# Kernel tuning notes

Hardware: AMD Instinct MI355X
Metric: run time of the kernel (lower is better)

## Reference

```python
import jax, jax.numpy as jnp
import numpy as np

N = 100000   # nodes
E = 1600000  # edges
B = 64       # graphs
NI, EI, GI = 64, 32, 32   # node_in, edge_in, global_in
NO, EO, GO = 32, 32, 32   # node_out, edge_out, global_out
H = 3                     # attention heads
NEG_SLOPE = 0.2


def setup_inputs() -> dict:
    key = jax.random.key(0)
    ks = jax.random.split(key, 20)
    s = 0.1
    return {
        # graph data
        "x": jax.random.normal(ks[0], (N, NI), jnp.float32),
        "edge_attr": jax.random.normal(ks[1], (E, EI), jnp.float32),
        "glob": jax.random.normal(ks[2], (B, GI), jnp.float32),
        # edge_mlp: Lin(node_in+edge_in, edge_out)
        "W_edge": jax.random.normal(ks[3], (NI + EI, EO), jnp.float32) * s,
        "b_edge": jax.random.normal(ks[4], (EO,), jnp.float32) * s,
        # GATv2Conv params (heads=3, edge_dim=EO)
        "W_l": jax.random.normal(ks[5], (NI, H * NO), jnp.float32) * s,
        "b_l": jax.random.normal(ks[6], (H * NO,), jnp.float32) * s,
        "W_r": jax.random.normal(ks[7], (NI, H * NO), jnp.float32) * s,
        "b_r": jax.random.normal(ks[8], (H * NO,), jnp.float32) * s,
        "W_e": jax.random.normal(ks[9], (EO, H * NO), jnp.float32) * s,   # lin_edge (no bias)
        "att": jax.random.normal(ks[10], (H, NO), jnp.float32) * s,
        "bias_gat": jax.random.normal(ks[11], (H * NO,), jnp.float32) * s,
        # node_mlp_2: Lin(node_out*3 + global_in, node_out)
        "W_n2": jax.random.normal(ks[12], (H * NO + GI, NO), jnp.float32) * s,
        "b_n2": jax.random.normal(ks[13], (NO,), jnp.float32) * s,
        # global_mlp: Lin(global_in + node_out, global_out)
        "W_g": jax.random.normal(ks[14], (GI + NO, GO), jnp.float32) * s,
        "b_g": jax.random.normal(ks[15], (GO,), jnp.float32) * s,
        # int inputs
        "edge_index": jax.random.randint(ks[16], (2, E), 0, N, jnp.int32),
        "batch": jnp.sort(jax.random.randint(ks[17], (N,), 0, B, jnp.int32)),
    }


def reference(x, edge_attr, glob, W_edge, b_edge, W_l, b_l, W_r, b_r, W_e,
              att, bias_gat, W_n2, b_n2, W_g, b_g, edge_index, batch):
    src, dst = edge_index[0], edge_index[1]

    # --- edge model: relu(Lin([x[src], edge_attr])) ---
    e = jax.nn.relu(jnp.concatenate([x[src], edge_attr], axis=1) @ W_edge + b_edge)  # [E, EO]

    # --- node model: GATv2Conv(heads=3, edge_dim=EO), concat heads ---
    xl = (x @ W_l + b_l).reshape(N, H, NO)   # source transform
    xr = (x @ W_r + b_r).reshape(N, H, NO)   # target transform
    m = xl[src] + xr[dst] + (e @ W_e).reshape(E, H, NO)          # [E,H,NO]
    logits = (jax.nn.leaky_relu(m, NEG_SLOPE) * att).sum(-1)     # [E,H]
    # segment softmax over incoming edges of each target node
    mx = jax.ops.segment_max(logits, dst, num_segments=N)        # [N,H]
    ex = jnp.exp(logits - mx[dst])
    den = jax.ops.segment_sum(ex, dst, num_segments=N)           # [N,H]
    alpha = ex / den[dst]                                        # [E,H]
    msg = (alpha[..., None] * xl[src]).reshape(E, H * NO)
    gat_out = jax.ops.segment_sum(msg, dst, num_segments=N) + bias_gat  # [N, H*NO]
    x_new = jax.nn.relu(jnp.concatenate([gat_out, glob[batch]], axis=1) @ W_n2 + b_n2)  # [N,NO]

    # --- global model: relu(Lin([glob, scatter_mean(x_new, batch)])) ---
    cnt = jax.ops.segment_sum(jnp.ones((N,), x.dtype), batch, num_segments=B)
    mean = jax.ops.segment_sum(x_new, batch, num_segments=B) / jnp.maximum(cnt, 1.0)[:, None]
    u_new = jax.nn.relu(jnp.concatenate([glob, mean], axis=1) @ W_g + b_g)  # [B,GO]

    return x_new, e, u_new
```

## Files before the change

### kernel.cpp

```cpp
#include <hip/hip_runtime.h>

#define N_NODES 100000
#define N_EDGES 1600000
#define NB 64
#define NI 64
#define EI 32
#define GI 32
#define NO 32
#define EO 32
#define GO 32
#define HH 3
#define HNO 96
#define NEG 0.2f
#define SCAN_BLKS 98

__global__ __launch_bounds__(256) void kA_node(
    const float* __restrict__ x,
    const float* __restrict__ W_l, const float* __restrict__ b_l,
    const float* __restrict__ W_r, const float* __restrict__ b_r,
    const float* __restrict__ W_edge, const float* __restrict__ b_edge,
    float* __restrict__ xl, float* __restrict__ xr, float* __restrict__ pre_e,
    int niters)
{
    __shared__ float sWl[NI * HNO];
    __shared__ float sWr[NI * HNO];
    __shared__ float sWp[NI * 32];
    __shared__ float sx[64 * NI];
    int t = threadIdx.x;
    for (int f = t; f < NI * HNO; f += 256) { sWl[f] = W_l[f]; sWr[f] = W_r[f]; }
    for (int f = t; f < NI * 32; f += 256) sWp[f] = W_edge[f];
    __syncthreads();
    int k = t & 31, g = t >> 5;
    float bl0 = b_l[k], bl1 = b_l[k + 32], bl2 = b_l[k + 64];
    float br0 = b_r[k], br1 = b_r[k + 32], br2 = b_r[k + 64];
    float bpe = b_edge[k];
    const long NX = (long)N_NODES * NI;
    for (int it = 0; it < niters; ++it) {
        long nb = ((long)blockIdx.x + (long)it * gridDim.x) * 64;
        long base = nb * NI;
        for (int f = t; f < 64 * NI; f += 256) {
            long idx = base + f;
            sx[f] = x[idx < NX ? idx : 0];
        }
        __syncthreads();
        float aL0[8], aL1[8], aL2[8], aR0[8], aR1[8], aR2[8], aP[8];
        #pragma unroll
        for (int m = 0; m < 8; ++m) {
            aL0[m] = bl0; aL1[m] = bl1; aL2[m] = bl2;
            aR0[m] = br0; aR1[m] = br1; aR2[m] = br2;
            aP[m] = bpe;
        }
        const float* sxg = &sx[g * 8 * NI];
        for (int i = 0; i < NI; ++i) {
            float wl0 = sWl[i * HNO + k], wl1 = sWl[i * HNO + 32 + k], wl2 = sWl[i * HNO + 64 + k];
            float wr0 = sWr[i * HNO + k], wr1 = sWr[i * HNO + 32 + k], wr2 = sWr[i * HNO + 64 + k];
            float wp  = sWp[i * 32 + k];
            #pragma unroll
            for (int m = 0; m < 8; ++m) {
                float xv = sxg[m * NI + i];
                aL0[m] += xv * wl0; aL1[m] += xv * wl1; aL2[m] += xv * wl2;
                aR0[m] += xv * wr0; aR1[m] += xv * wr1; aR2[m] += xv * wr2;
                aP[m]  += xv * wp;
            }
        }
        #pragma unroll
        for (int m = 0; m < 8; ++m) {
            long n = nb + g * 8 + m;
            if (n < N_NODES) {
                xl[n * HNO + k]      = aL0[m];
                xl[n * HNO + 32 + k] = aL1[m];
                xl[n * HNO + 64 + k] = aL2[m];
                xr[n * HNO + k]      = aR0[m];
                xr[n * HNO + 32 + k] = aR1[m];
                xr[n * HNO + 64 + k] = aR2[m];
                pre_e[n * 32 + k]    = aP[m];
            }
        }
        __syncthreads();
    }
}

__global__ __launch_bounds__(256) void k_hist(const int* __restrict__ eidx, int* __restrict__ cnt)
{
    long i = (long)blockIdx.x * 256 + threadIdx.x;
    long stride = (long)gridDim.x * 256;
    for (; i < N_EDGES; i += stride)
        atomicAdd(&cnt[eidx[N_EDGES + i]], 1);
}

__global__ __launch_bounds__(1024) void k_scan1(const int* __restrict__ cnt, int* __restrict__ bsum)
{
    __shared__ int s[1024];
    int i = blockIdx.x * 1024 + threadIdx.x;
    s[threadIdx.x] = (i < N_NODES) ? cnt[i] : 0;
    for (int o = 512; o > 0; o >>= 1) {
        __syncthreads();
        if (threadIdx.x < o) s[threadIdx.x] += s[threadIdx.x + o];
    }
    if (threadIdx.x == 0) bsum[blockIdx.x] = s[0];
}

__global__ __launch_bounds__(128) void k_scan2(int* __restrict__ bsum)
{
    __shared__ int s[128];
    int v = (threadIdx.x < SCAN_BLKS) ? bsum[threadIdx.x] : 0;
    s[threadIdx.x] = v;
    for (int o = 1; o < 128; o <<= 1) {
        __syncthreads();
        int a = (threadIdx.x >= o) ? s[threadIdx.x - o] : 0;
        __syncthreads();
        s[threadIdx.x] += a;
    }
    if (threadIdx.x < SCAN_BLKS) bsum[threadIdx.x] = s[threadIdx.x] - v;
}

__global__ __launch_bounds__(1024) void k_scan3(const int* __restrict__ cnt,
                                                const int* __restrict__ bsum,
                                                int* __restrict__ off, int* __restrict__ cursor)
{
    __shared__ int s[1024];
    int i = blockIdx.x * 1024 + threadIdx.x;
    int v = (i < N_NODES) ? cnt[i] : 0;
    s[threadIdx.x] = v;
    for (int o = 1; o < 1024; o <<= 1) {
        __syncthreads();
        int a = (threadIdx.x >= o) ? s[threadIdx.x - o] : 0;
        __syncthreads();
        s[threadIdx.x] += a;
    }
    int excl = bsum[blockIdx.x] + s[threadIdx.x] - v;
    if (i < N_NODES) {
        off[i] = excl; cursor[i] = excl;
        if (i == N_NODES - 1) off[N_NODES] = excl + v;
    }
}

__global__ __launch_bounds__(256) void k_scatter(const int* __restrict__ eidx,
                                                 int* __restrict__ cursor,
                                                 int2* __restrict__ ep)
{
    long i = (long)blockIdx.x * 256 + threadIdx.x;
    long stride = (long)gridDim.x * 256;
    for (; i < N_EDGES; i += stride) {
        int s = eidx[i];
        int d = eidx[N_EDGES + i];
        int pos = atomicAdd(&cursor[d], 1);
        ep[pos] = make_int2((int)i, s);
    }
}

__global__ __launch_bounds__(256) void kF(
    const float* __restrict__ pre_e, const float* __restrict__ ea,
    const float* __restrict__ W_edge, const float* __restrict__ W_e,
    const float* __restrict__ att,
    const float* __restrict__ xl, const float* __restrict__ xr,
    const int2* __restrict__ ep, const int* __restrict__ off,
    const float* __restrict__ bias_gat,
    float* __restrict__ e_out, float* __restrict__ g_out, int niters)
{
    __shared__ float sW2[32 * 32];
    __shared__ float sWe[32 * 96];
    __shared__ float2 sEa2[8][32];
    __shared__ float2 sEo2[8][32];
    int t = threadIdx.x;
    for (int f = t; f < 32 * 32; f += 256) sW2[f] = W_edge[64 * 32 + f];
    for (int f = t; f < 32 * 96; f += 256) sWe[f] = W_e[f];
    __syncthreads();
    int k = t & 31, gid = t >> 5;
    float at0 = att[k], at1 = att[32 + k], at2 = att[64 + k];
    float bg0 = bias_gat[k], bg1 = bias_gat[32 + k], bg2 = bias_gat[64 + k];
    for (int it = 0; it < niters; ++it) {
        long n = ((long)blockIdx.x + (long)it * gridDim.x) * 8 + gid;
        if (n >= N_NODES) continue;
        int lo = off[n], hi = off[n + 1];
        float xr0 = xr[n * HNO + k];
        float xr1 = xr[n * HNO + 32 + k];
        float xr2 = xr[n * HNO + 64 + k];
        float a0 = 0.f, a1 = 0.f, a2 = 0.f;
        float d0 = 0.f, d1 = 0.f, d2 = 0.f;
        int deg = hi - lo;
        int steps = (deg + 1) >> 1;
        int eA = 0, sA = 0, eB = 0, sB = 0;
        int eA1 = 0, sA1 = 0, eB1 = 0, sB1 = 0;
        float peA = 0.f, peB = 0.f, eaA = 0.f, eaB = 0.f;
        float xlA0 = 0.f, xlA1 = 0.f, xlA2 = 0.f, xlB0 = 0.f, xlB1 = 0.f, xlB2 = 0.f;
        if (steps > 0) {
            int2 q = ep[lo]; eA = q.x; sA = q.y;
            if (lo + 1 < hi) { int2 r = ep[lo + 1]; eB = r.x; sB = r.y; }
            peA = pre_e[(long)sA * 32 + k];   peB = pre_e[(long)sB * 32 + k];
            eaA = ea[(long)eA * EI + k];      eaB = ea[(long)eB * EI + k];
            xlA0 = xl[(long)sA * HNO + k]; xlA1 = xl[(long)sA * HNO + 32 + k]; xlA2 = xl[(long)sA * HNO + 64 + k];
            xlB0 = xl[(long)sB * HNO + k]; xlB1 = xl[(long)sB * HNO + 32 + k]; xlB2 = xl[(long)sB * HNO + 64 + k];
            if (lo + 2 < hi) { int2 q1 = ep[lo + 2]; eA1 = q1.x; sA1 = q1.y; }
            if (lo + 3 < hi) { int2 r1 = ep[lo + 3]; eB1 = r1.x; sB1 = r1.y; }
        }
        for (int st = 0; st < steps; ++st) {
            float peA_n = pre_e[(long)sA1 * 32 + k], peB_n = pre_e[(long)sB1 * 32 + k];
            float eaA_n = ea[(long)eA1 * EI + k],    eaB_n = ea[(long)eB1 * EI + k];
            float xlA0n = xl[(long)sA1 * HNO + k], xlA1n = xl[(long)sA1 * HNO + 32 + k], xlA2n = xl[(long)sA1 * HNO + 64 + k];
            float xlB0n = xl[(long)sB1 * HNO + k], xlB1n = xl[(long)sB1 * HNO + 32 + k], xlB2n = xl[(long)sB1 * HNO + 64 + k];
            int eA2 = 0, sA2 = 0, eB2 = 0, sB2 = 0;
            int pA2 = lo + 2 * st + 4;
            if (pA2 < hi)     { int2 q2 = ep[pA2];     eA2 = q2.x; sA2 = q2.y; }
            if (pA2 + 1 < hi) { int2 r2 = ep[pA2 + 1]; eB2 = r2.x; sB2 = r2.y; }
            sEa2[gid][k] = make_float2(eaA, eaB);
            float accA = peA, accB = peB;
            #pragma unroll 8
            for (int i = 0; i < 32; ++i) {
                float2 ev = sEa2[gid][i];
                float w = sW2[i * 32 + k];
                accA += ev.x * w; accB += ev.y * w;
            }
            float eoA = fmaxf(accA, 0.f), eoB = fmaxf(accB, 0.f);
            bool okB = (lo + 2 * st + 1) < hi;
            e_out[(long)eA * EO + k] = eoA;
            if (okB) e_out[(long)eB * EO + k] = eoB;
            sEo2[gid][k] = make_float2(eoA, eoB);
            float hA0 = xlA0 + xr0, hA1 = xlA1 + xr1, hA2 = xlA2 + xr2;
            float hB0 = xlB0 + xr0, hB1 = xlB1 + xr1, hB2 = xlB2 + xr2;
            #pragma unroll 8
            for (int i = 0; i < 32; ++i) {
                float2 ov = sEo2[gid][i];
                float w0 = sWe[i * 96 + k], w1 = sWe[i * 96 + 32 + k], w2 = sWe[i * 96 + 64 + k];
                hA0 += ov.x * w0; hA1 += ov.x * w1; hA2 += ov.x * w2;
                hB0 += ov.y * w0; hB1 += ov.y * w1; hB2 += ov.y * w2;
            }
            float pA0 = (hA0 > 0.f ? hA0 : NEG * hA0) * at0;
            float pA1 = (hA1 > 0.f ? hA1 : NEG * hA1) * at1;
            float pA2v = (hA2 > 0.f ? hA2 : NEG * hA2) * at2;
            float pB0 = (hB0 > 0.f ? hB0 : NEG * hB0) * at0;
            float pB1 = (hB1 > 0.f ? hB1 : NEG * hB1) * at1;
            float pB2 = (hB2 > 0.f ? hB2 : NEG * hB2) * at2;
            #pragma unroll
            for (int m = 1; m <= 16; m <<= 1) {
                pA0 += __shfl_xor(pA0, m, 32); pA1 += __shfl_xor(pA1, m, 32); pA2v += __shfl_xor(pA2v, m, 32);
                pB0 += __shfl_xor(pB0, m, 32); pB1 += __shfl_xor(pB1, m, 32); pB2 += __shfl_xor(pB2, m, 32);
            }
            float exA0 = __expf(pA0), exA1 = __expf(pA1), exA2 = __expf(pA2v);
            float exB0 = 0.f, exB1 = 0.f, exB2 = 0.f;
            if (okB) { exB0 = __expf(pB0); exB1 = __expf(pB1); exB2 = __expf(pB2); }
            a0 += exA0 * xlA0; a1 += exA1 * xlA1; a2 += exA2 * xlA2;
            a0 += exB0 * xlB0; a1 += exB1 * xlB1; a2 += exB2 * xlB2;
            d0 += exA0 + exB0; d1 += exA1 + exB1; d2 += exA2 + exB2;
            eA = eA1; sA = sA1; eB = eB1; sB = sB1;
            eA1 = eA2; sA1 = sA2; eB1 = eB2; sB1 = sB2;
            peA = peA_n; peB = peB_n; eaA = eaA_n; eaB = eaB_n;
            xlA0 = xlA0n; xlA1 = xlA1n; xlA2 = xlA2n;
            xlB0 = xlB0n; xlB1 = xlB1n; xlB2 = xlB2n;
        }
        g_out[n * HNO + k]      = (d0 > 0.f ? a0 / d0 : 0.f) + bg0;
        g_out[n * HNO + 32 + k] = (d1 > 0.f ? a1 / d1 : 0.f) + bg1;
        g_out[n * HNO + 64 + k] = (d2 > 0.f ? a2 / d2 : 0.f) + bg2;
    }
}

__global__ __launch_bounds__(256) void k2_node_out(
    const float* __restrict__ g, const float* __restrict__ glob,
    const int* __restrict__ batch, const float* __restrict__ W_n2,
    const float* __restrict__ b_n2, float* __restrict__ x_new, int niters)
{
    __shared__ float sW[128 * 32];
    __shared__ float sIn[8][128];
    int t = threadIdx.x;
    for (int f = t; f < 128 * 32; f += 256) sW[f] = W_n2[f];
    __syncthreads();
    int k = t & 31, ni = t >> 5;
    float bn = b_n2[k];
    for (int it = 0; it < niters; ++it) {
        long n = ((long)blockIdx.x + (long)it * gridDim.x) * 8 + ni;
        long nc = (n < N_NODES) ? n : 0;
        #pragma unroll
        for (int r = 0; r < 3; ++r) {
            int j = r * 32 + k;
            sIn[ni][j] = g[nc * HNO + j];
        }
        sIn[ni][96 + k] = glob[(long)batch[nc] * GI + k];
        __syncthreads();
        float acc = bn;
        #pragma unroll 8
        for (int i = 0; i < 128; ++i) acc += sIn[ni][i] * sW[i * 32 + k];
        if (n < N_NODES) x_new[n * NO + k] = fmaxf(acc, 0.f);
        __syncthreads();
    }
}

__device__ __forceinline__ int lower_bound_dev(const int* __restrict__ a, int n, int v) {
    int lo = 0, hi = n;
    while (lo < hi) { int mid = (lo + hi) >> 1; if (a[mid] < v) lo = mid + 1; else hi = mid; }
    return lo;
}

__global__ __launch_bounds__(256) void k3_global(
    const float* __restrict__ x_new, const int* __restrict__ batch,
    const float* __restrict__ glob, const float* __restrict__ W_g,
    const float* __restrict__ b_g, float* __restrict__ u_new)
{
    __shared__ int s_lo, s_hi;
    __shared__ float s_part[8][32];
    __shared__ float s_mean[32];
    int g = blockIdx.x;
    if (threadIdx.x == 0) {
        s_lo = lower_bound_dev(batch, N_NODES, g);
        s_hi = lower_bound_dev(batch, N_NODES, g + 1);
    }
    __syncthreads();
    int lo = s_lo, hi = s_hi;
    int k = threadIdx.x & 31, c = threadIdx.x >> 5;
    float acc = 0.f;
    for (long n = lo + c; n < hi; n += 8) acc += x_new[n * NO + k];
    s_part[c][k] = acc;
    __syncthreads();
    if (threadIdx.x < 32) {
        float s = 0.f;
        #pragma unroll
        for (int c2 = 0; c2 < 8; ++c2) s += s_part[c2][k];
        int cnt = hi - lo;
        s_mean[k] = s / (float)(cnt > 0 ? cnt : 1);
    }
    __syncthreads();
    if (threadIdx.x < 32) {
        float acc2 = b_g[k];
        #pragma unroll
        for (int i = 0; i < 32; ++i) acc2 += glob[g * GI + i] * W_g[i * GO + k];
        #pragma unroll
        for (int i = 0; i < 32; ++i) acc2 += s_mean[i] * W_g[(32 + i) * GO + k];
        u_new[g * GO + k] = fmaxf(acc2, 0.f);
    }
}

extern "C" void kernel_launch(void* const* d_in, const int* in_sizes, int n_in,
                              void* d_out, int out_size, void* d_ws, size_t ws_size,
                              hipStream_t stream) {
    const float* x        = (const float*)d_in[0];
    const float* edge_attr= (const float*)d_in[1];
    const float* glob     = (const float*)d_in[2];
    const float* W_edge   = (const float*)d_in[3];
    const float* b_edge   = (const float*)d_in[4];
    const float* W_l      = (const float*)d_in[5];
    const float* b_l      = (const float*)d_in[6];
    const float* W_r      = (const float*)d_in[7];
    const float* b_r      = (const float*)d_in[8];
    const float* W_e      = (const float*)d_in[9];
    const float* att      = (const float*)d_in[10];
    const float* bias_gat = (const float*)d_in[11];
    const float* W_n2     = (const float*)d_in[12];
    const float* b_n2     = (const float*)d_in[13];
    const float* W_g      = (const float*)d_in[14];
    const float* b_g      = (const float*)d_in[15];
    const int* edge_index = (const int*)d_in[16];
    const int* batch      = (const int*)d_in[17];

    float* out   = (float*)d_out;
    float* x_new = out;
    float* e_out = out + (size_t)N_NODES * NO;
    float* u_new = e_out + (size_t)N_EDGES * EO;

    float*  ws    = (float*)d_ws;
    float*  xl    = ws;
    float*  xr    = xl + (size_t)N_NODES * HNO;
    float*  pre_e = xr + (size_t)N_NODES * HNO;
    float*  g_buf = pre_e + (size_t)N_NODES * 32;
    int2*   ep    = (int2*)(g_buf + (size_t)N_NODES * HNO);
    int*    cnt   = (int*)(ep + (size_t)N_EDGES);
    int*    off   = cnt + N_NODES;
    int*    cursor= off + N_NODES + 1;
    int*    bsum  = cursor + N_NODES;

    hipMemsetAsync(cnt, 0, (size_t)N_NODES * sizeof(int), stream);

    k_hist<<<1024, 256, 0, stream>>>(edge_index, cnt);
    k_scan1<<<SCAN_BLKS, 1024, 0, stream>>>(cnt, bsum);
    k_scan2<<<1, 128, 0, stream>>>(bsum);
    k_scan3<<<SCAN_BLKS, 1024, 0, stream>>>(cnt, bsum, off, cursor);
    k_scatter<<<1024, 256, 0, stream>>>(edge_index, cursor, ep);

    int gridA = 1024;
    int groups64 = (N_NODES + 63) / 64;
    int itA = (groups64 + gridA - 1) / gridA;
    kA_node<<<gridA, 256, 0, stream>>>(x, W_l, b_l, W_r, b_r, W_edge, b_edge,
                                       xl, xr, pre_e, itA);

    int gridF = 2048;
    int groups8 = (N_NODES + 7) / 8;
    int itF = (groups8 + gridF - 1) / gridF;
    kF<<<gridF, 256, 0, stream>>>(pre_e, edge_attr, W_edge, W_e, att, xl, xr,
                                  ep, off, bias_gat, e_out, g_buf, itF);

    int grid2 = 1024;
    int it2 = (groups8 + grid2 - 1) / grid2;
    k2_node_out<<<grid2, 256, 0, stream>>>(g_buf, glob, batch, W_n2, b_n2, x_new, it2);

    k3_global<<<NB, 256, 0, stream>>>(x_new, batch, glob, W_g, b_g, u_new);
}
```

Before: 1.261 ms.

## Fuse node-output MLP into GAT edge kernel and vectorize shared weight reads

The separate node-output linear kernel is folded into the end of the per-node GAT aggregation kernel, so the 96-wide attention result goes straight from registers to shared memory and is never written to or read back from a global buffer. The edge-MLP and lin_edge weights are stored transposed in shared memory with a padded pitch, and the inner dot products become float4 loads along k instead of scalar loads. The cost is about 16 KB more shared memory per block for the fused weights, which may lower occupancy in the gather-heavy edge loop. The fused 128-term matvec relies on each 32-lane group being its own lockstep unit, since no barrier is placed between writing and reading sG.

```diff
diff --git a/kernel.cpp b/kernel.cpp
--- a/kernel.cpp
+++ b/kernel.cpp
@@ -13,6 +13,7 @@
 #define HNO 96
 #define NEG 0.2f
 #define SCAN_BLKS 98
+#define WPITCH 36
 
 __global__ __launch_bounds__(256) void kA_node(
     const float* __restrict__ x,
@@ -155,20 +156,43 @@
     const float* __restrict__ att,
     const float* __restrict__ xl, const float* __restrict__ xr,
     const int2* __restrict__ ep, const int* __restrict__ off,
-    const float* __restrict__ bias_gat,
-    float* __restrict__ e_out, float* __restrict__ g_out, int niters)
-{
-    __shared__ float sW2[32 * 32];
-    __shared__ float sWe[32 * 96];
-    __shared__ float2 sEa2[8][32];
-    __shared__ float2 sEo2[8][32];
+    const float* __restrict__ bias_gat, const float* __restrict__ glob,
+    const int* __restrict__ batch, const float* __restrict__ W_n2,
+    const float* __restrict__ b_n2,
+    float* __restrict__ e_out, float* __restrict__ x_new, int niters)
+{
+    __shared__ __align__(16) float sW2T[32 * WPITCH];
+    __shared__ __align__(16) float sWeT[3][32 * WPITCH];
+    __shared__ __align__(16) float sEaA[8][32];
+    __shared__ __align__(16) float sEaB[8][32];
+    __shared__ __align__(16) float sEoA[8][32];
+    __shared__ __align__(16) float sEoB[8][32];
+    __shared__ float sWn[128 * 32];
+    __shared__ float sG[8][128];
     int t = threadIdx.x;
-    for (int f = t; f < 32 * 32; f += 256) sW2[f] = W_edge[64 * 32 + f];
-    for (int f = t; f < 32 * 96; f += 256) sWe[f] = W_e[f];
+    for (int f = t; f < 1024; f += 256) {
+        int kk = f >> 5, ii = f & 31;
+        sW2T[kk * WPITCH + ii] = W_edge[(64 + ii) * 32 + kk];
+    }
+    for (int f = t; f < 3072; f += 256) {
+        int h = f >> 10, r = f & 1023;
+        int kk = r >> 5, ii = r & 31;
+        sWeT[h][kk * WPITCH + ii] = W_e[ii * 96 + h * 32 + kk];
+    }
+    for (int f = t; f < 128 * 32; f += 256) sWn[f] = W_n2[f];
     __syncthreads();
     int k = t & 31, gid = t >> 5;
     float at0 = att[k], at1 = att[32 + k], at2 = att[64 + k];
     float bg0 = bias_gat[k], bg1 = bias_gat[32 + k], bg2 = bias_gat[64 + k];
+    float bn = b_n2[k];
+    const float4* w2p = (const float4*)&sW2T[k * WPITCH];
+    const float4* we0p = (const float4*)&sWeT[0][k * WPITCH];
+    const float4* we1p = (const float4*)&sWeT[1][k * WPITCH];
+    const float4* we2p = (const float4*)&sWeT[2][k * WPITCH];
+    const float4* eaAp = (const float4*)&sEaA[gid][0];
+    const float4* eaBp = (const float4*)&sEaB[gid][0];
+    const float4* eoAp = (const float4*)&sEoA[gid][0];
+    const float4* eoBp = (const float4*)&sEoB[gid][0];
     for (int it = 0; it < niters; ++it) {
         long n = ((long)blockIdx.x + (long)it * gridDim.x) * 8 + gid;
         if (n >= N_NODES) continue;
@@ -182,13 +206,13 @@
         int steps = (deg + 1) >> 1;
         int eA = 0, sA = 0, eB = 0, sB = 0;
         int eA1 = 0, sA1 = 0, eB1 = 0, sB1 = 0;
-        float peA = 0.f, peB = 0.f, eaA = 0.f, eaB = 0.f;
+        float peA = 0.f, peB = 0.f, eaAv = 0.f, eaBv = 0.f;
         float xlA0 = 0.f, xlA1 = 0.f, xlA2 = 0.f, xlB0 = 0.f, xlB1 = 0.f, xlB2 = 0.f;
         if (steps > 0) {
             int2 q = ep[lo]; eA = q.x; sA = q.y;
             if (lo + 1 < hi) { int2 r = ep[lo + 1]; eB = r.x; sB = r.y; }
             peA = pre_e[(long)sA * 32 + k];   peB = pre_e[(long)sB * 32 + k];
-            eaA = ea[(long)eA * EI + k];      eaB = ea[(long)eB * EI + k];
+            eaAv = ea[(long)eA * EI + k];     eaBv = ea[(long)eB * EI + k];
             xlA0 = xl[(long)sA * HNO + k]; xlA1 = xl[(long)sA * HNO + 32 + k]; xlA2 = xl[(long)sA * HNO + 64 + k];
             xlB0 = xl[(long)sB * HNO + k]; xlB1 = xl[(long)sB * HNO + 32 + k]; xlB2 = xl[(long)sB * HNO + 64 + k];
             if (lo + 2 < hi) { int2 q1 = ep[lo + 2]; eA1 = q1.x; sA1 = q1.y; }
@@ -203,27 +227,36 @@
             int pA2 = lo + 2 * st + 4;
             if (pA2 < hi)     { int2 q2 = ep[pA2];     eA2 = q2.x; sA2 = q2.y; }
             if (pA2 + 1 < hi) { int2 r2 = ep[pA2 + 1]; eB2 = r2.x; sB2 = r2.y; }
-            sEa2[gid][k] = make_float2(eaA, eaB);
+            sEaA[gid][k] = eaAv;
+            sEaB[gid][k] = eaBv;
             float accA = peA, accB = peB;
-            #pragma unroll 8
-            for (int i = 0; i < 32; ++i) {
-                float2 ev = sEa2[gid][i];
-                float w = sW2[i * 32 + k];
-                accA += ev.x * w; accB += ev.y * w;
+            #pragma unroll
+            for (int i4 = 0; i4 < 8; ++i4) {
+                float4 w  = w2p[i4];
+                float4 a4 = eaAp[i4];
+                float4 b4 = eaBp[i4];
+                accA += a4.x * w.x + a4.y * w.y + a4.z * w.z + a4.w * w.w;
+                accB += b4.x * w.x + b4.y * w.y + b4.z * w.z + b4.w * w.w;
             }
             float eoA = fmaxf(accA, 0.f), eoB = fmaxf(accB, 0.f);
             bool okB = (lo + 2 * st + 1) < hi;
             e_out[(long)eA * EO + k] = eoA;
             if (okB) e_out[(long)eB * EO + k] = eoB;
-            sEo2[gid][k] = make_float2(eoA, eoB);
+            sEoA[gid][k] = eoA;
+            sEoB[gid][k] = eoB;
             float hA0 = xlA0 + xr0, hA1 = xlA1 + xr1, hA2 = xlA2 + xr2;
             float hB0 = xlB0 + xr0, hB1 = xlB1 + xr1, hB2 = xlB2 + xr2;
-            #pragma unroll 8
-            for (int i = 0; i < 32; ++i) {
-                float2 ov = sEo2[gid][i];
-                float w0 = sWe[i * 96 + k], w1 = sWe[i * 96 + 32 + k], w2 = sWe[i * 96 + 64 + k];
-                hA0 += ov.x * w0; hA1 += ov.x * w1; hA2 += ov.x * w2;
-                hB0 += ov.y * w0; hB1 += ov.y * w1; hB2 += ov.y * w2;
+            #pragma unroll
+            for (int i4 = 0; i4 < 8; ++i4) {
+                float4 oA = eoAp[i4];
+                float4 oB = eoBp[i4];
+                float4 w0 = we0p[i4], w1 = we1p[i4], w2v = we2p[i4];
+                hA0 += oA.x * w0.x + oA.y * w0.y + oA.z * w0.z + oA.w * w0.w;
+                hA1 += oA.x * w1.x + oA.y * w1.y + oA.z * w1.z + oA.w * w1.w;
+                hA2 += oA.x * w2v.x + oA.y * w2v.y + oA.z * w2v.z + oA.w * w2v.w;
+                hB0 += oB.x * w0.x + oB.y * w0.y + oB.z * w0.z + oB.w * w0.w;
+                hB1 += oB.x * w1.x + oB.y * w1.y + oB.z * w1.z + oB.w * w1.w;
+                hB2 += oB.x * w2v.x + oB.y * w2v.y + oB.z * w2v.z + oB.w * w2v.w;
             }
             float pA0 = (hA0 > 0.f ? hA0 : NEG * hA0) * at0;
             float pA1 = (hA1 > 0.f ? hA1 : NEG * hA1) * at1;
@@ -244,43 +277,19 @@
             d0 += exA0 + exB0; d1 += exA1 + exB1; d2 += exA2 + exB2;
             eA = eA1; sA = sA1; eB = eB1; sB = sB1;
             eA1 = eA2; sA1 = sA2; eB1 = eB2; sB1 = sB2;
-            peA = peA_n; peB = peB_n; eaA = eaA_n; eaB = eaB_n;
+            peA = peA_n; peB = peB_n; eaAv = eaA_n; eaBv = eaB_n;
             xlA0 = xlA0n; xlA1 = xlA1n; xlA2 = xlA2n;
             xlB0 = xlB0n; xlB1 = xlB1n; xlB2 = xlB2n;
         }
-        g_out[n * HNO + k]      = (d0 > 0.f ? a0 / d0 : 0.f) + bg0;
-        g_out[n * HNO + 32 + k] = (d1 > 0.f ? a1 / d1 : 0.f) + bg1;
-        g_out[n * HNO + 64 + k] = (d2 > 0.f ? a2 / d2 : 0.f) + bg2;
-    }
-}
-
-__global__ __launch_bounds__(256) void k2_node_out(
-    const float* __restrict__ g, const float* __restrict__ glob,
-    const int* __restrict__ batch, const float* __restrict__ W_n2,
-    const float* __restrict__ b_n2, float* __restrict__ x_new, int niters)
-{
-    __shared__ float sW[128 * 32];
-    __shared__ float sIn[8][128];
-    int t = threadIdx.x;
-    for (int f = t; f < 128 * 32; f += 256) sW[f] = W_n2[f];
-    __syncthreads();
-    int k = t & 31, ni = t >> 5;
-    float bn = b_n2[k];
-    for (int it = 0; it < niters; ++it) {
-        long n = ((long)blockIdx.x + (long)it * gridDim.x) * 8 + ni;
-        long nc = (n < N_NODES) ? n : 0;
-        #pragma unroll
-        for (int r = 0; r < 3; ++r) {
-            int j = r * 32 + k;
-            sIn[ni][j] = g[nc * HNO + j];
-        }
-        sIn[ni][96 + k] = glob[(long)batch[nc] * GI + k];
-        __syncthreads();
-        float acc = bn;
+        float g0 = (d0 > 0.f ? a0 / d0 : 0.f) + bg0;
+        float g1 = (d1 > 0.f ? a1 / d1 : 0.f) + bg1;
+        float g2 = (d2 > 0.f ? a2 / d2 : 0.f) + bg2;
+        float gg = glob[(long)batch[n] * GI + k];
+        sG[gid][k] = g0; sG[gid][32 + k] = g1; sG[gid][64 + k] = g2; sG[gid][96 + k] = gg;
+        float acc2 = bn;
         #pragma unroll 8
-        for (int i = 0; i < 128; ++i) acc += sIn[ni][i] * sW[i * 32 + k];
-        if (n < N_NODES) x_new[n * NO + k] = fmaxf(acc, 0.f);
-        __syncthreads();
+        for (int i = 0; i < 128; ++i) acc2 += sG[gid][i] * sWn[i * 32 + k];
+        x_new[n * NO + k] = fmaxf(acc2, 0.f);
     }
 }
 
@@ -359,8 +368,7 @@
     float*  xl    = ws;
     float*  xr    = xl + (size_t)N_NODES * HNO;
     float*  pre_e = xr + (size_t)N_NODES * HNO;
-    float*  g_buf = pre_e + (size_t)N_NODES * 32;
-    int2*   ep    = (int2*)(g_buf + (size_t)N_NODES * HNO);
+    int2*   ep    = (int2*)(pre_e + (size_t)N_NODES * 32);
     int*    cnt   = (int*)(ep + (size_t)N_EDGES);
     int*    off   = cnt + N_NODES;
     int*    cursor= off + N_NODES + 1;
@@ -384,11 +392,8 @@
     int groups8 = (N_NODES + 7) / 8;
     int itF = (groups8 + gridF - 1) / gridF;
     kF<<<gridF, 256, 0, stream>>>(pre_e, edge_attr, W_edge, W_e, att, xl, xr,
-                                  ep, off, bias_gat, e_out, g_buf, itF);
-
-    int grid2 = 1024;
-    int it2 = (groups8 + grid2 - 1) / grid2;
-    k2_node_out<<<grid2, 256, 0, stream>>>(g_buf, glob, batch, W_n2, b_n2, x_new, it2);
+                                  ep, off, bias_gat, glob, batch, W_n2, b_n2,
+                                  e_out, x_new, itF);
 
     k3_global<<<NB, 256, 0, stream>>>(x_new, batch, glob, W_g, b_g, u_new);
 }
```

New measurement: 1.838 ms. +45.8%, slower.

## Split edge MLP out of GAT kernel and co-schedule it with CSR scatter

Applied to the files above, without the earlier changes.

The edge MLP (relu of pre_e[src] plus edge_attr times W_edge) moves out of the per-destination GAT kernel into a separate edge-ordered pass. That pass shares one launch with the CSR scatter, using disjoint block ranges so the scatter atomics and the dense edge compute run concurrently. The GAT kernel then reads the finished e_out gathered by edge id instead of recomputing it, which drops the random pre_e and edge_attr gathers and the inner 32x32 matmul from its hot loop. The cost is writing e_out and then reading it back randomly: one extra 205MB gather pass instead of two 205MB-ish random gathers.

```diff
diff --git a/kernel.cpp b/kernel.cpp
--- a/kernel.cpp
+++ b/kernel.cpp
@@ -13,6 +13,8 @@
 #define HNO 96
 #define NEG 0.2f
 #define SCAN_BLKS 98
+#define SCAT_BLKS 1024
+#define KE_BLKS 2048
 
 __global__ __launch_bounds__(256) void kA_node(
     const float* __restrict__ x,
@@ -135,35 +137,54 @@
     }
 }
 
-__global__ __launch_bounds__(256) void k_scatter(const int* __restrict__ eidx,
-                                                 int* __restrict__ cursor,
-                                                 int2* __restrict__ ep)
-{
-    long i = (long)blockIdx.x * 256 + threadIdx.x;
-    long stride = (long)gridDim.x * 256;
-    for (; i < N_EDGES; i += stride) {
-        int s = eidx[i];
-        int d = eidx[N_EDGES + i];
-        int pos = atomicAdd(&cursor[d], 1);
-        ep[pos] = make_int2((int)i, s);
+__global__ __launch_bounds__(256) void k_scat_ke(
+    const int* __restrict__ eidx, int* __restrict__ cursor, int2* __restrict__ ep,
+    const float* __restrict__ pre_e, const float* __restrict__ ea,
+    const float* __restrict__ W_edge, float* __restrict__ e_out)
+{
+    __shared__ float sW2[32 * 32];
+    __shared__ float sEa[8][32];
+    int t = threadIdx.x;
+    if (blockIdx.x < SCAT_BLKS) {
+        long i = (long)blockIdx.x * 256 + t;
+        long stride = (long)SCAT_BLKS * 256;
+        for (; i < N_EDGES; i += stride) {
+            int s = eidx[i];
+            int d = eidx[N_EDGES + i];
+            int pos = atomicAdd(&cursor[d], 1);
+            ep[pos] = make_int2((int)i, s);
+        }
+    } else {
+        int bid = blockIdx.x - SCAT_BLKS;
+        for (int f = t; f < 32 * 32; f += 256) sW2[f] = W_edge[64 * 32 + f];
+        __syncthreads();
+        int k = t & 31, gid = t >> 5;
+        const int niters = (N_EDGES + KE_BLKS * 8 - 1) / (KE_BLKS * 8);
+        for (int it = 0; it < niters; ++it) {
+            long e = ((long)bid + (long)it * KE_BLKS) * 8 + gid;
+            bool valid = (e < N_EDGES);
+            long ec = valid ? e : 0;
+            int s = eidx[ec];
+            float acc = pre_e[(long)s * 32 + k];
+            sEa[gid][k] = ea[ec * EI + k];
+            #pragma unroll 8
+            for (int i = 0; i < 32; ++i) acc += sEa[gid][i] * sW2[i * 32 + k];
+            if (valid) e_out[ec * EO + k] = fmaxf(acc, 0.f);
+        }
     }
 }
 
 __global__ __launch_bounds__(256) void kF(
-    const float* __restrict__ pre_e, const float* __restrict__ ea,
-    const float* __restrict__ W_edge, const float* __restrict__ W_e,
+    const float* __restrict__ eo_in, const float* __restrict__ W_e,
     const float* __restrict__ att,
     const float* __restrict__ xl, const float* __restrict__ xr,
     const int2* __restrict__ ep, const int* __restrict__ off,
     const float* __restrict__ bias_gat,
-    float* __restrict__ e_out, float* __restrict__ g_out, int niters)
-{
-    __shared__ float sW2[32 * 32];
+    float* __restrict__ g_out, int niters)
+{
     __shared__ float sWe[32 * 96];
-    __shared__ float2 sEa2[8][32];
     __shared__ float2 sEo2[8][32];
     int t = threadIdx.x;
-    for (int f = t; f < 32 * 32; f += 256) sW2[f] = W_edge[64 * 32 + f];
     for (int f = t; f < 32 * 96; f += 256) sWe[f] = W_e[f];
     __syncthreads();
     int k = t & 31, gid = t >> 5;
@@ -182,48 +203,36 @@
         int steps = (deg + 1) >> 1;
         int eA = 0, sA = 0, eB = 0, sB = 0;
         int eA1 = 0, sA1 = 0, eB1 = 0, sB1 = 0;
-        float peA = 0.f, peB = 0.f, eaA = 0.f, eaB = 0.f;
+        float eoAc = 0.f, eoBc = 0.f;
         float xlA0 = 0.f, xlA1 = 0.f, xlA2 = 0.f, xlB0 = 0.f, xlB1 = 0.f, xlB2 = 0.f;
         if (steps > 0) {
             int2 q = ep[lo]; eA = q.x; sA = q.y;
             if (lo + 1 < hi) { int2 r = ep[lo + 1]; eB = r.x; sB = r.y; }
-            peA = pre_e[(long)sA * 32 + k];   peB = pre_e[(long)sB * 32 + k];
-            eaA = ea[(long)eA * EI + k];      eaB = ea[(long)eB * EI + k];
+            eoAc = eo_in[(long)eA * EO + k];
+            eoBc = eo_in[(long)eB * EO + k];
             xlA0 = xl[(long)sA * HNO + k]; xlA1 = xl[(long)sA * HNO + 32 + k]; xlA2 = xl[(long)sA * HNO + 64 + k];
             xlB0 = xl[(long)sB * HNO + k]; xlB1 = xl[(long)sB * HNO + 32 + k]; xlB2 = xl[(long)sB * HNO + 64 + k];
             if (lo + 2 < hi) { int2 q1 = ep[lo + 2]; eA1 = q1.x; sA1 = q1.y; }
             if (lo + 3 < hi) { int2 r1 = ep[lo + 3]; eB1 = r1.x; sB1 = r1.y; }
         }
         for (int st = 0; st < steps; ++st) {
-            float peA_n = pre_e[(long)sA1 * 32 + k], peB_n = pre_e[(long)sB1 * 32 + k];
-            float eaA_n = ea[(long)eA1 * EI + k],    eaB_n = ea[(long)eB1 * EI + k];
+            float eoA_n = eo_in[(long)eA1 * EO + k];
+            float eoB_n = eo_in[(long)eB1 * EO + k];
             float xlA0n = xl[(long)sA1 * HNO + k], xlA1n = xl[(long)sA1 * HNO + 32 + k], xlA2n = xl[(long)sA1 * HNO + 64 + k];
             float xlB0n = xl[(long)sB1 * HNO + k], xlB1n = xl[(long)sB1 * HNO + 32 + k], xlB2n = xl[(long)sB1 * HNO + 64 + k];
             int eA2 = 0, sA2 = 0, eB2 = 0, sB2 = 0;
             int pA2 = lo + 2 * st + 4;
             if (pA2 < hi)     { int2 q2 = ep[pA2];     eA2 = q2.x; sA2 = q2.y; }
             if (pA2 + 1 < hi) { int2 r2 = ep[pA2 + 1]; eB2 = r2.x; sB2 = r2.y; }
-            sEa2[gid][k] = make_float2(eaA, eaB);
-            float accA = peA, accB = peB;
-            #pragma unroll 8
-            for (int i = 0; i < 32; ++i) {
-                float2 ev = sEa2[gid][i];
-                float w = sW2[i * 32 + k];
-                accA += ev.x * w; accB += ev.y * w;
-            }
-            float eoA = fmaxf(accA, 0.f), eoB = fmaxf(accB, 0.f);
-            bool okB = (lo + 2 * st + 1) < hi;
-            e_out[(long)eA * EO + k] = eoA;
-            if (okB) e_out[(long)eB * EO + k] = eoB;
-            sEo2[gid][k] = make_float2(eoA, eoB);
+            sEo2[gid][k] = make_float2(eoAc, eoBc);
             float hA0 = xlA0 + xr0, hA1 = xlA1 + xr1, hA2 = xlA2 + xr2;
             float hB0 = xlB0 + xr0, hB1 = xlB1 + xr1, hB2 = xlB2 + xr2;
             #pragma unroll 8
             for (int i = 0; i < 32; ++i) {
                 float2 ov = sEo2[gid][i];
-                float w0 = sWe[i * 96 + k], w1 = sWe[i * 96 + 32 + k], w2 = sWe[i * 96 + 64 + k];
-                hA0 += ov.x * w0; hA1 += ov.x * w1; hA2 += ov.x * w2;
-                hB0 += ov.y * w0; hB1 += ov.y * w1; hB2 += ov.y * w2;
+                float w0 = sWe[i * 96 + k], w1 = sWe[i * 96 + 32 + k], w2v = sWe[i * 96 + 64 + k];
+                hA0 += ov.x * w0; hA1 += ov.x * w1; hA2 += ov.x * w2v;
+                hB0 += ov.y * w0; hB1 += ov.y * w1; hB2 += ov.y * w2v;
             }
             float pA0 = (hA0 > 0.f ? hA0 : NEG * hA0) * at0;
             float pA1 = (hA1 > 0.f ? hA1 : NEG * hA1) * at1;
@@ -236,6 +245,7 @@
                 pA0 += __shfl_xor(pA0, m, 32); pA1 += __shfl_xor(pA1, m, 32); pA2v += __shfl_xor(pA2v, m, 32);
                 pB0 += __shfl_xor(pB0, m, 32); pB1 += __shfl_xor(pB1, m, 32); pB2 += __shfl_xor(pB2, m, 32);
             }
+            bool okB = (lo + 2 * st + 1) < hi;
             float exA0 = __expf(pA0), exA1 = __expf(pA1), exA2 = __expf(pA2v);
             float exB0 = 0.f, exB1 = 0.f, exB2 = 0.f;
             if (okB) { exB0 = __expf(pB0); exB1 = __expf(pB1); exB2 = __expf(pB2); }
@@ -244,7 +254,7 @@
             d0 += exA0 + exB0; d1 += exA1 + exB1; d2 += exA2 + exB2;
             eA = eA1; sA = sA1; eB = eB1; sB = sB1;
             eA1 = eA2; sA1 = sA2; eB1 = eB2; sB1 = sB2;
-            peA = peA_n; peB = peB_n; eaA = eaA_n; eaB = eaB_n;
+            eoAc = eoA_n; eoBc = eoB_n;
             xlA0 = xlA0n; xlA1 = xlA1n; xlA2 = xlA2n;
             xlB0 = xlB0n; xlB1 = xlB1n; xlB2 = xlB2n;
         }
@@ -372,7 +382,6 @@
     k_scan1<<<SCAN_BLKS, 1024, 0, stream>>>(cnt, bsum);
     k_scan2<<<1, 128, 0, stream>>>(bsum);
     k_scan3<<<SCAN_BLKS, 1024, 0, stream>>>(cnt, bsum, off, cursor);
-    k_scatter<<<1024, 256, 0, stream>>>(edge_index, cursor, ep);
 
     int gridA = 1024;
     int groups64 = (N_NODES + 63) / 64;
@@ -380,11 +389,14 @@
     kA_node<<<gridA, 256, 0, stream>>>(x, W_l, b_l, W_r, b_r, W_edge, b_edge,
                                        xl, xr, pre_e, itA);
 
+    k_scat_ke<<<SCAT_BLKS + KE_BLKS, 256, 0, stream>>>(edge_index, cursor, ep,
+                                                       pre_e, edge_attr, W_edge, e_out);
+
     int gridF = 2048;
     int groups8 = (N_NODES + 7) / 8;
     int itF = (groups8 + gridF - 1) / gridF;
-    kF<<<gridF, 256, 0, stream>>>(pre_e, edge_attr, W_edge, W_e, att, xl, xr,
-                                  ep, off, bias_gat, e_out, g_buf, itF);
+    kF<<<gridF, 256, 0, stream>>>(e_out, W_e, att, xl, xr,
+                                  ep, off, bias_gat, g_buf, itF);
 
     int grid2 = 1024;
     int it2 = (groups8 + grid2 - 1) / grid2;
```

Result: slower. 1.343 ms (+6.5%).
